# Performance work log

Hardware: AMD Instinct MI355X
Metric: run time of the kernel (lower is better)

The kernel has to match this reference:

```python
import jax, jax.numpy as jnp
import numpy as np

B, T, C, H = 8, 2048, 1024, 64  # batch, block_size(=seq), embedding_dim, head_size

def setup_inputs() -> dict:
    key = jax.random.key(0)
    kx, kk, kq, kv = jax.random.split(key, 4)
    s = 1.0 / np.sqrt(C)
    return {
        "x": jax.random.normal(kx, (B, T, C), dtype=jnp.float32),
        "Wk": jax.random.normal(kk, (C, H), dtype=jnp.float32) * s,
        "Wq": jax.random.normal(kq, (C, H), dtype=jnp.float32) * s,
        "Wv": jax.random.normal(kv, (C, H), dtype=jnp.float32) * s,
    }

def reference(x, Wk, Wq, Wv):
    # projections: [B,T,C] @ [C,H] -> [B,T,H]
    k = jnp.einsum("btc,ch->bth", x, Wk)
    q = jnp.einsum("btc,ch->bth", x, Wq)
    v = jnp.einsum("btc,ch->bth", x, Wv)
    # scores: [B,T,T], scaled by head_size^-0.5
    wei = jnp.einsum("bth,bsh->bts", q, k) * (k.shape[-1] ** -0.5)
    # causal mask (lower-triangular keep)
    causal = jnp.tril(jnp.ones((T, T), dtype=bool))
    wei = jnp.where(causal[None, :, :], wei, -jnp.inf)
    wei = jax.nn.softmax(wei, axis=-1)
    # dropout_rate=0.0 -> identity
    out = jnp.einsum("bts,bsh->bth", wei, v)
    return out
```

## Files before the change

### kernel.cpp

```cpp
#include <hip/hip_runtime.h>

#define NB 8
#define NT 2048
#define NC 1024
#define NH 64
#define BT (NB*NT)

typedef __bf16 bf16x8 __attribute__((ext_vector_type(8)));
typedef float  f32x4  __attribute__((ext_vector_type(4)));
typedef unsigned short us8 __attribute__((ext_vector_type(8)));

__device__ __forceinline__ unsigned short f2bf(float f) {
  unsigned u = __builtin_bit_cast(unsigned, f);
  u = (u + 0x7FFFu + ((u >> 16) & 1u)) >> 16;
  return (unsigned short)u;
}

__device__ __forceinline__ bf16x8 ld_frag(const unsigned short* p) {
  return __builtin_bit_cast(bf16x8, *(const us8*)p);
}

__global__ __launch_bounds__(256) void wconv_kernel(
    const float* __restrict__ Wk, const float* __restrict__ Wq,
    const float* __restrict__ Wv, unsigned short* __restrict__ Wt)
{
  __shared__ unsigned short T[64][72];
  const int t = threadIdx.x;
  const int mat = blockIdx.x >> 4;
  const int k0 = (blockIdx.x & 15) * 64;
  const float* __restrict__ W = (mat == 0) ? Wq : (mat == 1) ? Wk : Wv;
  const int kk = t >> 2, h0 = (t & 3) * 16;
  const float* src = &W[(size_t)(k0 + kk) * NH + h0];
#pragma unroll
  for (int j = 0; j < 4; ++j) {
    const float4 v = *(const float4*)(src + j*4);
    T[h0 + j*4 + 0][kk] = f2bf(v.x);
    T[h0 + j*4 + 1][kk] = f2bf(v.y);
    T[h0 + j*4 + 2][kk] = f2bf(v.z);
    T[h0 + j*4 + 3][kk] = f2bf(v.w);
  }
  __syncthreads();
  const int h = t >> 2, c0 = (t & 3) * 16;
  unsigned short* dst = &Wt[(size_t)(mat*64 + h) * NC + k0 + c0];
  *(us8*)dst       = *(const us8*)&T[h][c0];
  *(us8*)(dst + 8) = *(const us8*)&T[h][c0 + 8];
}

__global__ __launch_bounds__(256) void proj_kernel(
    const float* __restrict__ x, const unsigned short* __restrict__ Wt,
    unsigned short* __restrict__ qkv)
{
  __shared__ unsigned short Vb[4][64][18];

  const int t = threadIdx.x, w = t >> 6, lane = t & 63;
  const int W = blockIdx.x * 4 + w;
  const int row0 = (W >> 1) * 16;
  const int cb = (W & 1) * 96;
  const int fr = lane & 15, fo = (lane >> 4) * 8, rg = (lane >> 4) * 4;

  f32x4 acc[6];
#pragma unroll
  for (int n = 0; n < 6; ++n) acc[n] = (f32x4){0.f, 0.f, 0.f, 0.f};

  const float* __restrict__ xrow = &x[(size_t)(row0 + fr) * NC];

  for (int k0 = 0; k0 < NC; k0 += 64) {
    bf16x8 af[2];
#pragma unroll
    for (int ks = 0; ks < 2; ++ks) {
      const float* p = xrow + k0 + ks*32 + fo;
      const float4 a = *(const float4*)p;
      const float4 b = *(const float4*)(p + 4);
      bf16x8 v;
      v[0] = (__bf16)a.x; v[1] = (__bf16)a.y; v[2] = (__bf16)a.z; v[3] = (__bf16)a.w;
      v[4] = (__bf16)b.x; v[5] = (__bf16)b.y; v[6] = (__bf16)b.z; v[7] = (__bf16)b.w;
      af[ks] = v;
    }
    bf16x8 bfr[2][6];
#pragma unroll
    for (int ks = 0; ks < 2; ++ks)
#pragma unroll
      for (int n = 0; n < 6; ++n)
        bfr[ks][n] = ld_frag(&Wt[(size_t)(cb + n*16 + fr) * NC + k0 + ks*32 + fo]);
#pragma unroll
    for (int ks = 0; ks < 2; ++ks)
#pragma unroll
      for (int n = 0; n < 6; ++n)
        acc[n] = __builtin_amdgcn_mfma_f32_16x16x32_bf16(af[ks], bfr[ks][n], acc[n], 0, 0, 0);
  }

#pragma unroll
  for (int n = 0; n < 6; ++n) {
    const int col = cb + n*16;
    if (col < 128) {
      const int mat = col >> 6;
      unsigned short* op = qkv + (size_t)mat * BT * NH;
      const int h = (col & 63) + fr;
#pragma unroll
      for (int r = 0; r < 4; ++r)
        op[(size_t)(row0 + rg + r) * NH + h] = f2bf(acc[n][r]);
    } else {
#pragma unroll
      for (int r = 0; r < 4; ++r)
        Vb[w][(col - 128) + fr][rg + r] = f2bf(acc[n][r]);
    }
  }
  if (cb == 96) {
    unsigned short* vt = qkv + (size_t)2 * BT * NH;
    unsigned short* dst = &vt[(size_t)lane * BT + row0];
    *(us8*)dst       = *(const us8*)&Vb[w][lane][0];
    *(us8*)(dst + 8) = *(const us8*)&Vb[w][lane][8];
  }
}

__global__ __launch_bounds__(256) void attn_kernel(
    const unsigned short* __restrict__ qkv, float* __restrict__ out)
{
  __shared__ unsigned short Psm[4][16][72];
  __shared__ float co[4][16][68];
  __shared__ float cl[4][16];

  const int t = threadIdx.x, w = t >> 6, lane = t & 63;
  const int lin = blockIdx.x + 64 * blockIdx.y;
  const int b = lin & 7;
  const int j0 = lin >> 3;
  const unsigned short* __restrict__ qp = qkv;
  const unsigned short* __restrict__ kp = qkv + (size_t)BT * NH;
  const unsigned short* __restrict__ vt = qkv + (size_t)2 * BT * NH;
  const int fr = lane & 15, fo = (lane >> 4) * 8, rg = (lane >> 4) * 4;

#pragma unroll 1
  for (int ph = 0; ph < 2; ++ph) {
    const int j = ph ? (127 - j0) : j0;
    const int q0 = j * 16;
    const int ntiles = (j >> 2) + 1;

    bf16x8 aq0, aq1;
    {
      const size_t qoff = ((size_t)b * NT + q0 + fr) * NH;
      aq0 = ld_frag(&qp[qoff + fo]);
      aq1 = ld_frag(&qp[qoff + 32 + fo]);
    }

    f32x4 o[4];
#pragma unroll
    for (int n = 0; n < 4; ++n) o[n] = (f32x4){0.f, 0.f, 0.f, 0.f};
    float lp[4] = {0.f, 0.f, 0.f, 0.f};

    for (int kt = w; kt < ntiles; kt += 4) {
      const int kv0 = kt * 64;

      f32x4 s[4];
#pragma unroll
      for (int n = 0; n < 4; ++n) s[n] = (f32x4){0.f, 0.f, 0.f, 0.f};
#pragma unroll
      for (int n = 0; n < 4; ++n) {
        const size_t koff = ((size_t)b*NT + kv0 + n*16 + fr) * NH + fo;
        s[n] = __builtin_amdgcn_mfma_f32_16x16x32_bf16(aq0, ld_frag(&kp[koff]), s[n], 0, 0, 0);
        s[n] = __builtin_amdgcn_mfma_f32_16x16x32_bf16(aq1, ld_frag(&kp[koff + 32]), s[n], 0, 0, 0);
      }

#pragma unroll
      for (int n = 0; n < 4; ++n)
#pragma unroll
        for (int r = 0; r < 4; ++r) s[n][r] = __expf(s[n][r] * 0.125f);

      if (kt == ntiles - 1) {
#pragma unroll
        for (int n = 0; n < 4; ++n) {
          const int col = kv0 + n*16 + fr;
#pragma unroll
          for (int r = 0; r < 4; ++r)
            if (col > q0 + rg + r) s[n][r] = 0.f;
        }
      }

#pragma unroll
      for (int r = 0; r < 4; ++r)
        lp[r] += (s[0][r] + s[1][r]) + (s[2][r] + s[3][r]);

#pragma unroll
      for (int n = 0; n < 4; ++n)
#pragma unroll
        for (int r = 0; r < 4; ++r)
          Psm[w][rg + r][n*16 + fr] = f2bf(s[n][r]);

      bf16x8 pa0 = ld_frag(&Psm[w][fr][fo]);
      bf16x8 pa1 = ld_frag(&Psm[w][fr][32 + fo]);

#pragma unroll
      for (int n = 0; n < 4; ++n) {
        const size_t voff = (size_t)(n*16 + fr) * BT + (size_t)b*NT + kv0 + fo;
        o[n] = __builtin_amdgcn_mfma_f32_16x16x32_bf16(pa0, ld_frag(&vt[voff]), o[n], 0, 0, 0);
        o[n] = __builtin_amdgcn_mfma_f32_16x16x32_bf16(pa1, ld_frag(&vt[voff + 32]), o[n], 0, 0, 0);
      }
    }

#pragma unroll
    for (int r = 0; r < 4; ++r) {
#pragma unroll
      for (int off = 1; off < 16; off <<= 1) lp[r] += __shfl_xor(lp[r], off);
    }
    if (fr == 0) {
#pragma unroll
      for (int r = 0; r < 4; ++r) cl[w][rg + r] = lp[r];
    }
#pragma unroll
    for (int n = 0; n < 4; ++n)
#pragma unroll
      for (int r = 0; r < 4; ++r) co[w][rg + r][n*16 + fr] = o[n][r];
    __syncthreads();

    {
      const int row = t >> 4, c0 = (t & 15) * 4;
      const float l = (cl[0][row] + cl[1][row]) + (cl[2][row] + cl[3][row]);
      const float inv = 1.f / l;
      float4 ov;
      ov.x = ((co[0][row][c0+0] + co[1][row][c0+0]) + (co[2][row][c0+0] + co[3][row][c0+0])) * inv;
      ov.y = ((co[0][row][c0+1] + co[1][row][c0+1]) + (co[2][row][c0+1] + co[3][row][c0+1])) * inv;
      ov.z = ((co[0][row][c0+2] + co[1][row][c0+2]) + (co[2][row][c0+2] + co[3][row][c0+2])) * inv;
      ov.w = ((co[0][row][c0+3] + co[1][row][c0+3]) + (co[2][row][c0+3] + co[3][row][c0+3])) * inv;
      *(float4*)&out[((size_t)b*NT + q0 + row) * NH + c0] = ov;
    }
    if (ph == 0) __syncthreads();
  }
}

extern "C" void kernel_launch(void* const* d_in, const int* in_sizes, int n_in,
                              void* d_out, int out_size, void* d_ws, size_t ws_size,
                              hipStream_t stream) {
  (void)in_sizes; (void)n_in; (void)out_size; (void)ws_size;
  const float* x  = (const float*)d_in[0];
  const float* Wk = (const float*)d_in[1];
  const float* Wq = (const float*)d_in[2];
  const float* Wv = (const float*)d_in[3];
  unsigned short* qkv = (unsigned short*)d_ws;
  unsigned short* Wt  = qkv + (size_t)3 * BT * NH;

  wconv_kernel<<<48, 256, 0, stream>>>(Wk, Wq, Wv, Wt);
  proj_kernel<<<BT/32, 256, 0, stream>>>(x, Wt, qkv);
  attn_kernel<<<dim3(64, NB), 256, 0, stream>>>(qkv, (float*)d_out);
}
```

Before: 184.6 us.

## Stage x tile in LDS for shared reuse in projection; use 8 waves in attention

The projection kernel now loads a 32x64 fp32 tile of x once per block into shared memory. All four waves reuse it, each computing 48 output columns for 32 rows, instead of each wave reading x from global on its own (the old layout read each x row twice). This cuts global traffic on x at the cost of two barriers per k-step. The attention kernel moves from 4 to 8 waves per block, splitting key tiles across more waves for more parallelism per query tile, with a wider final reduction over 8 partial accumulators.

```diff
diff --git a/kernel.cpp b/kernel.cpp
--- a/kernel.cpp
+++ b/kernel.cpp
@@ -50,75 +50,89 @@
     const float* __restrict__ x, const unsigned short* __restrict__ Wt,
     unsigned short* __restrict__ qkv)
 {
-  __shared__ unsigned short Vb[4][64][18];
+  __shared__ float Asmf[32][68];
+  __shared__ unsigned short Vb[64][40];
 
   const int t = threadIdx.x, w = t >> 6, lane = t & 63;
-  const int W = blockIdx.x * 4 + w;
-  const int row0 = (W >> 1) * 16;
-  const int cb = (W & 1) * 96;
+  const int m0 = blockIdx.x * 32;
   const int fr = lane & 15, fo = (lane >> 4) * 8, rg = (lane >> 4) * 4;
 
-  f32x4 acc[6];
-#pragma unroll
-  for (int n = 0; n < 6; ++n) acc[n] = (f32x4){0.f, 0.f, 0.f, 0.f};
-
-  const float* __restrict__ xrow = &x[(size_t)(row0 + fr) * NC];
+  f32x4 acc[2][3];
+#pragma unroll
+  for (int m = 0; m < 2; ++m)
+#pragma unroll
+    for (int n = 0; n < 3; ++n) acc[m][n] = (f32x4){0.f, 0.f, 0.f, 0.f};
+
+  const int srow0 = t >> 4, scol = (t & 15) * 4;
+  const int srow1 = srow0 + 16;
 
   for (int k0 = 0; k0 < NC; k0 += 64) {
-    bf16x8 af[2];
-#pragma unroll
-    for (int ks = 0; ks < 2; ++ks) {
-      const float* p = xrow + k0 + ks*32 + fo;
-      const float4 a = *(const float4*)p;
-      const float4 b = *(const float4*)(p + 4);
-      bf16x8 v;
-      v[0] = (__bf16)a.x; v[1] = (__bf16)a.y; v[2] = (__bf16)a.z; v[3] = (__bf16)a.w;
-      v[4] = (__bf16)b.x; v[5] = (__bf16)b.y; v[6] = (__bf16)b.z; v[7] = (__bf16)b.w;
-      af[ks] = v;
-    }
-    bf16x8 bfr[2][6];
+    {
+      const float4 a = *(const float4*)&x[(size_t)(m0 + srow0) * NC + k0 + scol];
+      const float4 b = *(const float4*)&x[(size_t)(m0 + srow1) * NC + k0 + scol];
+      *(f32x4*)&Asmf[srow0][scol] = (f32x4){a.x, a.y, a.z, a.w};
+      *(f32x4*)&Asmf[srow1][scol] = (f32x4){b.x, b.y, b.z, b.w};
+    }
+    __syncthreads();
+
+    bf16x8 af[2][2], bfr[2][3];
+#pragma unroll
+    for (int m = 0; m < 2; ++m)
+#pragma unroll
+      for (int ks = 0; ks < 2; ++ks) {
+        const f32x4 lo = *(const f32x4*)&Asmf[m*16 + fr][ks*32 + fo];
+        const f32x4 hi = *(const f32x4*)&Asmf[m*16 + fr][ks*32 + fo + 4];
+        bf16x8 v;
+        v[0] = (__bf16)lo[0]; v[1] = (__bf16)lo[1]; v[2] = (__bf16)lo[2]; v[3] = (__bf16)lo[3];
+        v[4] = (__bf16)hi[0]; v[5] = (__bf16)hi[1]; v[6] = (__bf16)hi[2]; v[7] = (__bf16)hi[3];
+        af[m][ks] = v;
+      }
 #pragma unroll
     for (int ks = 0; ks < 2; ++ks)
 #pragma unroll
-      for (int n = 0; n < 6; ++n)
-        bfr[ks][n] = ld_frag(&Wt[(size_t)(cb + n*16 + fr) * NC + k0 + ks*32 + fo]);
+      for (int n = 0; n < 3; ++n)
+        bfr[ks][n] = ld_frag(&Wt[(size_t)(w*48 + n*16 + fr) * NC + k0 + ks*32 + fo]);
 #pragma unroll
     for (int ks = 0; ks < 2; ++ks)
 #pragma unroll
-      for (int n = 0; n < 6; ++n)
-        acc[n] = __builtin_amdgcn_mfma_f32_16x16x32_bf16(af[ks], bfr[ks][n], acc[n], 0, 0, 0);
-  }
-
-#pragma unroll
-  for (int n = 0; n < 6; ++n) {
-    const int col = cb + n*16;
-    if (col < 128) {
-      const int mat = col >> 6;
-      unsigned short* op = qkv + (size_t)mat * BT * NH;
-      const int h = (col & 63) + fr;
-#pragma unroll
-      for (int r = 0; r < 4; ++r)
-        op[(size_t)(row0 + rg + r) * NH + h] = f2bf(acc[n][r]);
-    } else {
-#pragma unroll
-      for (int r = 0; r < 4; ++r)
-        Vb[w][(col - 128) + fr][rg + r] = f2bf(acc[n][r]);
-    }
-  }
-  if (cb == 96) {
+      for (int m = 0; m < 2; ++m)
+#pragma unroll
+        for (int n = 0; n < 3; ++n)
+          acc[m][n] = __builtin_amdgcn_mfma_f32_16x16x32_bf16(af[m][ks], bfr[ks][n], acc[m][n], 0, 0, 0);
+    __syncthreads();
+  }
+
+#pragma unroll
+  for (int m = 0; m < 2; ++m)
+#pragma unroll
+    for (int n = 0; n < 3; ++n) {
+      const int col = w*48 + n*16;
+      if (col < 128) {
+        unsigned short* op = qkv + (size_t)(col >> 6) * BT * NH;
+        const int h = (col & 63) + fr;
+#pragma unroll
+        for (int r = 0; r < 4; ++r)
+          op[(size_t)(m0 + m*16 + rg + r) * NH + h] = f2bf(acc[m][n][r]);
+      } else {
+#pragma unroll
+        for (int r = 0; r < 4; ++r)
+          Vb[(col - 128) + fr][m*16 + rg + r] = f2bf(acc[m][n][r]);
+      }
+    }
+  __syncthreads();
+  {
     unsigned short* vt = qkv + (size_t)2 * BT * NH;
-    unsigned short* dst = &vt[(size_t)lane * BT + row0];
-    *(us8*)dst       = *(const us8*)&Vb[w][lane][0];
-    *(us8*)(dst + 8) = *(const us8*)&Vb[w][lane][8];
-  }
-}
-
-__global__ __launch_bounds__(256) void attn_kernel(
+    const int h = t >> 2, c = (t & 3) * 8;
+    *(us8*)&vt[(size_t)h * BT + m0 + c] = *(const us8*)&Vb[h][c];
+  }
+}
+
+__global__ __launch_bounds__(512) void attn_kernel(
     const unsigned short* __restrict__ qkv, float* __restrict__ out)
 {
-  __shared__ unsigned short Psm[4][16][72];
-  __shared__ float co[4][16][68];
-  __shared__ float cl[4][16];
+  __shared__ unsigned short Psm[8][16][72];
+  __shared__ float co[8][16][68];
+  __shared__ float cl[8][16];
 
   const int t = threadIdx.x, w = t >> 6, lane = t & 63;
   const int lin = blockIdx.x + 64 * blockIdx.y;
@@ -147,7 +161,7 @@
     for (int n = 0; n < 4; ++n) o[n] = (f32x4){0.f, 0.f, 0.f, 0.f};
     float lp[4] = {0.f, 0.f, 0.f, 0.f};
 
-    for (int kt = w; kt < ntiles; kt += 4) {
+    for (int kt = w; kt < ntiles; kt += 8) {
       const int kv0 = kt * 64;
 
       f32x4 s[4];
@@ -212,15 +226,21 @@
     __syncthreads();
 
     {
-      const int row = t >> 4, c0 = (t & 15) * 4;
-      const float l = (cl[0][row] + cl[1][row]) + (cl[2][row] + cl[3][row]);
-      const float inv = 1.f / l;
-      float4 ov;
-      ov.x = ((co[0][row][c0+0] + co[1][row][c0+0]) + (co[2][row][c0+0] + co[3][row][c0+0])) * inv;
-      ov.y = ((co[0][row][c0+1] + co[1][row][c0+1]) + (co[2][row][c0+1] + co[3][row][c0+1])) * inv;
-      ov.z = ((co[0][row][c0+2] + co[1][row][c0+2]) + (co[2][row][c0+2] + co[3][row][c0+2])) * inv;
-      ov.w = ((co[0][row][c0+3] + co[1][row][c0+3]) + (co[2][row][c0+3] + co[3][row][c0+3])) * inv;
-      *(float4*)&out[((size_t)b*NT + q0 + row) * NH + c0] = ov;
+      const int row = (t >> 4) & 15, c0 = (t & 15) * 4;
+      if (t < 256) {
+        float l = 0.f;
+#pragma unroll
+        for (int ww = 0; ww < 8; ++ww) l += cl[ww][row];
+        const float inv = 1.f / l;
+        float4 ov = {0.f, 0.f, 0.f, 0.f};
+#pragma unroll
+        for (int ww = 0; ww < 8; ++ww) {
+          ov.x += co[ww][row][c0+0]; ov.y += co[ww][row][c0+1];
+          ov.z += co[ww][row][c0+2]; ov.w += co[ww][row][c0+3];
+        }
+        ov.x *= inv; ov.y *= inv; ov.z *= inv; ov.w *= inv;
+        *(float4*)&out[((size_t)b*NT + q0 + row) * NH + c0] = ov;
+      }
     }
     if (ph == 0) __syncthreads();
   }
@@ -239,5 +259,5 @@
 
   wconv_kernel<<<48, 256, 0, stream>>>(Wk, Wq, Wv, Wt);
   proj_kernel<<<BT/32, 256, 0, stream>>>(x, Wt, qkv);
-  attn_kernel<<<dim3(64, NB), 256, 0, stream>>>(qkv, (float*)d_out);
-}
+  attn_kernel<<<dim3(64, NB), 512, 0, stream>>>(qkv, (float*)d_out);
+}
```

New measurement: 152.5 us. 17.4% less time.
